# Kernel tuning notes

Hardware: AMD Instinct MI355X
Metric: run time of the kernel (lower is better)

## Reference

```python
import jax, jax.numpy as jnp
import numpy as np

B, IN, H = 16384, 1024, 1024


def setup_inputs() -> dict:
    key = jax.random.key(0)
    ks = jax.random.split(key, 7)
    s_in = 1.0 / np.sqrt(IN)
    s_h = 1.0 / np.sqrt(H)
    return {
        "x": jax.random.normal(ks[0], (B, IN), jnp.float32),
        "h0": jax.random.normal(ks[1], (B, H), jnp.float32),
        "c0": jax.random.normal(ks[2], (B, H), jnp.float32),
        # gate order along leading dim: f, i, o, g
        "wi": jax.random.uniform(ks[3], (4, H, IN), jnp.float32, -s_in, s_in),
        "bi": jax.random.uniform(ks[4], (4, H), jnp.float32, -s_in, s_in),
        "wh": jax.random.uniform(ks[5], (4, H, H), jnp.float32, -s_h, s_h),
        "bh": jax.random.uniform(ks[6], (4, H), jnp.float32, -s_h, s_h),
    }


def reference(x, h0, c0, wi, bi, wh, bh):
    # pre-activations for all 4 gates in two fused GEMMs: [b, 4, h]
    z = (jnp.einsum("bi,ghi->bgh", x, wi) + bi
         + jnp.einsum("bj,ghj->bgh", h0, wh) + bh)
    f = jax.nn.sigmoid(z[:, 0])   # forget gate
    i = jax.nn.sigmoid(z[:, 1])   # input gate
    o = jax.nn.sigmoid(z[:, 2])   # output gate
    g = jnp.tanh(z[:, 3])         # candidates
    ct = f * c0 + i * g
    ht = o * jnp.tanh(ct)
    return ht, ct
```

## Files before the change

### kernel.cpp

```cpp
#include <hip/hip_runtime.h>
#include <hip/hip_bf16.h>
#include <stdint.h>

#define B_ROWS 16384
#define K_DIM  2048
#define H_DIM  1024
#define N_DIM  4096
#define KB     (K_DIM * 2)
#define NT     (K_DIM / 64)
#define BUFSZ  65536u

using f32x4   = __attribute__((ext_vector_type(4))) float;
using f32x16  = __attribute__((ext_vector_type(16))) float;
using bf16x8  = __attribute__((ext_vector_type(8))) __bf16;

__device__ __forceinline__ unsigned short f2bf(float f) {
    union { float f; unsigned u; } v; v.f = f;
    unsigned r = v.u + 0x7fffu + ((v.u >> 16) & 1u);
    return (unsigned short)(r >> 16);
}

__device__ __forceinline__ void gload16(const void* g, const void* l) {
    __builtin_amdgcn_global_load_lds(
        (const __attribute__((address_space(1))) void*)g,
        (__attribute__((address_space(3))) void*)l,
        16, 0, 0);
}

__device__ __forceinline__ float rcp1p(float e) {
    return __builtin_amdgcn_rcpf(1.f + e);
}

__global__ void pack_a_kernel(const float* __restrict__ x, const float* __restrict__ h0,
                              unsigned short* __restrict__ A) {
    int tid = blockIdx.x * 256 + threadIdx.x;
    int64_t idx = (int64_t)tid * 4;
    int b = (int)(idx >> 11);
    int k = (int)(idx & 2047);
    const float* src = (k < 1024) ? (x + (int64_t)b * 1024 + k)
                                  : (h0 + (int64_t)b * 1024 + (k - 1024));
    float4 v = *(const float4*)src;
    ushort4 o;
    o.x = f2bf(v.x); o.y = f2bf(v.y); o.z = f2bf(v.z); o.w = f2bf(v.w);
    *(ushort4*)(A + idx) = o;
}

__global__ void pack_w_kernel(const float* __restrict__ wi, const float* __restrict__ wh,
                              const float* __restrict__ bi, const float* __restrict__ bh,
                              unsigned short* __restrict__ W, float* __restrict__ bias) {
    int tid = blockIdx.x * 256 + threadIdx.x;
    int64_t idx = (int64_t)tid * 4;
    int r = (int)(idx >> 11);
    int k = (int)(idx & 2047);
    int h = r >> 2, g = r & 3;
    const float* src = (k < 1024)
        ? (wi + (int64_t)g * 1048576 + (int64_t)h * 1024 + k)
        : (wh + (int64_t)g * 1048576 + (int64_t)h * 1024 + (k - 1024));
    float4 v = *(const float4*)src;
    ushort4 o;
    o.x = f2bf(v.x); o.y = f2bf(v.y); o.z = f2bf(v.z); o.w = f2bf(v.w);
    *(ushort4*)(W + idx) = o;
    if (k == 0) bias[r] = bi[g * 1024 + h] + bh[g * 1024 + h];
}


#define SCHED0  __builtin_amdgcn_sched_barrier(0)
#define FENCE   asm volatile("" ::: "memory")
#define BAR     __builtin_amdgcn_s_barrier()

#define PH_PRE  do { FENCE; BAR; \
                     asm volatile("s_waitcnt lgkmcnt(0)" ::: "memory"); \
                     SCHED0; __builtin_amdgcn_s_setprio(1); } while (0)
#define PH_POST_V do { __builtin_amdgcn_s_setprio(0); SCHED0; \
                       asm volatile("s_waitcnt vmcnt(4)" ::: "memory"); \
                       SCHED0; FENCE; BAR; } while (0)

__global__ __launch_bounds__(512, 2) void lstm_gemm_fused(
    const unsigned short* __restrict__ A, const unsigned short* __restrict__ W,
    const float* __restrict__ bias, const float* __restrict__ c0,
    float* __restrict__ ht, float* __restrict__ ct)
{
    __shared__ char sm[131072];

    const int tid = threadIdx.x;
    const int l   = tid & 63;
    const int w   = tid >> 6;
    const int wm  = w >> 2;
    const int wn  = w & 3;

    const int bid = blockIdx.x;
    const int nid = (bid & 7) * 128 + (bid >> 3);
    const int bm  = nid >> 4;
    const int bn  = nid & 15;

    f32x16 acc[4][2];
#pragma unroll
    for (int i = 0; i < 4; ++i)
#pragma unroll
        for (int j = 0; j < 2; ++j)
#pragma unroll
            for (int e = 0; e < 16; ++e) acc[i][j][e] = 0.f;

    const int srow = w * 16 + (l >> 2);
    const int scb  = ((l & 3) << 4) ^ (l & 32);
    const char* Asrc = (const char*)A + (size_t)(bm * 256 + srow) * KB + scb;
    const char* Wsrc = (const char*)W + (size_t)(bn * 256 + srow) * KB + scb;
    const uint32_t wL = (uint32_t)w * 1024u;

#define STAGE_A(KK, BOFF) do { \
    gload16(Asrc + (KK) * 64,            sm + (BOFF) + (KK) * 16384u + wL); \
    gload16(Asrc + (KK) * 64 + 128 * KB, sm + (BOFF) + (KK) * 16384u + 8192u + wL); \
} while (0)
#define STAGE_B(KK, BOFF) do { \
    gload16(Wsrc + (KK) * 64,            sm + (BOFF) + 32768u + (KK) * 16384u + wL); \
    gload16(Wsrc + (KK) * 64 + 128 * KB, sm + (BOFF) + 32768u + (KK) * 16384u + 8192u + wL); \
} while (0)

    const uint32_t sub   = ((uint32_t)(l >> 4) & 1u) * 1024u;
    const uint32_t lofA  = (uint32_t)(l & 15) * 64u + ((uint32_t)(l >> 5)) * 16u;
    const uint32_t xr    = (uint32_t)((l & 8) << 2);
    const uint32_t lane0 = sub + lofA + xr;
    const uint32_t lane1 = sub + lofA + (xr ^ 32u);
    const uint32_t ArdB  = (uint32_t)wm * 8192u;
    const uint32_t BrdB  = 32768u + (uint32_t)wn * 4096u;

    bf16x8 af[4][2], bf[2][2];

#define RD_PHASE(BOFF, KK) do { \
    const uint32_t cb_ = (BOFF) + (KK) * 16384u; \
    _Pragma("unroll") \
    for (int mf_ = 0; mf_ < 4; ++mf_) { \
        af[mf_][0] = *(const bf16x8*)(sm + cb_ + ArdB + mf_ * 2048u + lane0); \
        af[mf_][1] = *(const bf16x8*)(sm + cb_ + ArdB + mf_ * 2048u + lane1); \
    } \
    _Pragma("unroll") \
    for (int nf_ = 0; nf_ < 2; ++nf_) { \
        bf[nf_][0] = *(const bf16x8*)(sm + cb_ + BrdB + nf_ * 2048u + lane0); \
        bf[nf_][1] = *(const bf16x8*)(sm + cb_ + BrdB + nf_ * 2048u + lane1); \
    } \
} while (0)

#define MFMA16 do { \
    _Pragma("unroll") \
    for (int ks_ = 0; ks_ < 2; ++ks_) \
        _Pragma("unroll") \
        for (int mf_ = 0; mf_ < 4; ++mf_) \
            _Pragma("unroll") \
            for (int nf_ = 0; nf_ < 2; ++nf_) \
                acc[mf_][nf_] = __builtin_amdgcn_mfma_f32_32x32x16_bf16( \
                    af[mf_][ks_], bf[nf_][ks_], acc[mf_][nf_], 0, 0, 0); \
} while (0)

    STAGE_A(0, 0u); STAGE_B(0, 0u);
    STAGE_A(1, 0u); STAGE_B(1, 0u);
    Asrc += 128; Wsrc += 128;
    asm volatile("s_waitcnt vmcnt(4)" ::: "memory");
    SCHED0; FENCE; BAR;

#define DO_TILE(CUR, NXT) do { \
     \
    RD_PHASE(CUR, 0); \
    STAGE_A(0, NXT); STAGE_B(0, NXT); \
    PH_PRE; MFMA16; PH_POST_V; \
     \
    RD_PHASE(CUR, 1); \
    STAGE_A(1, NXT); STAGE_B(1, NXT); \
    PH_PRE; MFMA16; PH_POST_V; \
    Asrc += 128; Wsrc += 128; \
} while (0)

#pragma unroll 1
    for (int tt = 0; tt < NT; tt += 2) {
        DO_TILE(0u, BUFSZ);
        DO_TILE(BUFSZ, 0u);
    }

    asm volatile("s_waitcnt vmcnt(0) lgkmcnt(0)" ::: "memory");
    FENCE; BAR;

    float* ep = (float*)(void*)sm + w * 2176;
    const int hbase = bn * 64 + wn * 16;
    const int rbase = bm * 256 + wm * 128;
    const int rl = (l >> 5) * 4;
    const int cl = l & 31;

#pragma unroll
    for (int mf = 0; mf < 4; ++mf) {
#pragma unroll
        for (int nf = 0; nf < 2; ++nf)
#pragma unroll
            for (int g = 0; g < 4; ++g)
#pragma unroll
                for (int ri = 0; ri < 4; ++ri)
                    ep[(ri + g * 8 + rl) * 68 + nf * 32 + cl] = acc[mf][nf][g * 4 + ri];

#pragma unroll
        for (int it = 0; it < 8; ++it) {
            const int c   = it * 64 + l;
            const int row = c >> 4;
            const int hq  = c & 15;
            f32x4 z = *(const f32x4*)(ep + row * 68 + hq * 4);
            const int hg = hbase + hq;
            const float4 bz = ((const float4*)bias)[hg];
            const int brow = rbase + mf * 32 + row;

            float zf = z.x + bz.x;
            float zi = z.y + bz.y;
            float zo = z.z + bz.z;
            float zg = z.w + bz.w;

            float fg = rcp1p(__expf(-zf));
            float ig = rcp1p(__expf(-zi));
            float og = rcp1p(__expf(-zo));
            float gg = 2.f * rcp1p(__expf(-2.f * zg)) - 1.f;

            int64_t oi = (int64_t)brow * H_DIM + hg;
            float cc = fg * c0[oi] + ig * gg;
            float hh = og * (2.f * rcp1p(__expf(-2.f * cc)) - 1.f);
            ct[oi] = cc;
            ht[oi] = hh;
        }
    }
}

extern "C" void kernel_launch(void* const* d_in, const int* in_sizes, int n_in,
                              void* d_out, int out_size, void* d_ws, size_t ws_size,
                              hipStream_t stream) {
    const float* x  = (const float*)d_in[0];
    const float* h0 = (const float*)d_in[1];
    const float* c0 = (const float*)d_in[2];
    const float* wi = (const float*)d_in[3];
    const float* bi = (const float*)d_in[4];
    const float* wh = (const float*)d_in[5];
    const float* bh = (const float*)d_in[6];

    float* ht = (float*)d_out;
    float* ct = ht + (int64_t)B_ROWS * H_DIM;

    char* ws = (char*)d_ws;
    unsigned short* A  = (unsigned short*)ws;
    unsigned short* Wp = (unsigned short*)(ws + (64u << 20));
    float*          bs = (float*)(ws + (80u << 20));

    pack_a_kernel<<<32768, 256, 0, stream>>>(x, h0, A);
    pack_w_kernel<<<8192, 256, 0, stream>>>(wi, wh, bi, bh, Wp, bs);

    lstm_gemm_fused<<<1024, 512, 0, stream>>>(A, Wp, bs, c0, ht, ct);
}
```

Baseline: 344.0 us.

## Software-pipeline LDS fragment reads against MFMA with double-buffered A registers

Restructures the GEMM main loop so the LDS reads for the next k-phase are issued before the MFMAs of the current phase. Two alternating A-fragment register sets (aX/aY) make this possible, and there is now one barrier per phase instead of two. The explicit sched_barrier and lgkmcnt waits are removed, and an explicit prologue and epilogue drain the pipeline. It also adds a wave-parity XOR to the LDS swizzle, applied to both the global-to-LDS stores and the fragment reads, to reduce bank conflicts. The costs are higher register pressure, and tighter barrier ordering between buffer reuse and in-flight reads.

```diff
diff --git a/kernel.cpp b/kernel.cpp
--- a/kernel.cpp
+++ b/kernel.cpp
@@ -8,7 +8,8 @@
 #define N_DIM  4096
 #define KB     (K_DIM * 2)
 #define NT     (K_DIM / 64)
-#define BUFSZ  65536u
+#define BUF0   0u
+#define BUF1   65536u
 
 using f32x4   = __attribute__((ext_vector_type(4))) float;
 using f32x16  = __attribute__((ext_vector_type(16))) float;
@@ -64,16 +65,11 @@
 }
 
 
-#define SCHED0  __builtin_amdgcn_sched_barrier(0)
-#define FENCE   asm volatile("" ::: "memory")
-#define BAR     __builtin_amdgcn_s_barrier()
-
-#define PH_PRE  do { FENCE; BAR; \
-                     asm volatile("s_waitcnt lgkmcnt(0)" ::: "memory"); \
-                     SCHED0; __builtin_amdgcn_s_setprio(1); } while (0)
-#define PH_POST_V do { __builtin_amdgcn_s_setprio(0); SCHED0; \
-                       asm volatile("s_waitcnt vmcnt(4)" ::: "memory"); \
-                       SCHED0; FENCE; BAR; } while (0)
+#define FENCE asm volatile("" ::: "memory")
+#define BAR   __builtin_amdgcn_s_barrier()
+#define VM4   asm volatile("s_waitcnt vmcnt(4)" ::: "memory")
+#define SP1   __builtin_amdgcn_s_setprio(1)
+#define SP0   __builtin_amdgcn_s_setprio(0)
 
 __global__ __launch_bounds__(512, 2) void lstm_gemm_fused(
     const unsigned short* __restrict__ A, const unsigned short* __restrict__ W,
@@ -102,45 +98,48 @@
             for (int e = 0; e < 16; ++e) acc[i][j][e] = 0.f;
 
     const int srow = w * 16 + (l >> 2);
-    const int scb  = ((l & 3) << 4) ^ (l & 32);
+    const int scb  = (((l & 3) << 4) ^ (l & 32)) ^ ((w & 1) << 4);
     const char* Asrc = (const char*)A + (size_t)(bm * 256 + srow) * KB + scb;
     const char* Wsrc = (const char*)W + (size_t)(bn * 256 + srow) * KB + scb;
     const uint32_t wL = (uint32_t)w * 1024u;
 
-#define STAGE_A(KK, BOFF) do { \
+#define STAGE_AB(KK, BOFF) do { \
     gload16(Asrc + (KK) * 64,            sm + (BOFF) + (KK) * 16384u + wL); \
     gload16(Asrc + (KK) * 64 + 128 * KB, sm + (BOFF) + (KK) * 16384u + 8192u + wL); \
-} while (0)
-#define STAGE_B(KK, BOFF) do { \
     gload16(Wsrc + (KK) * 64,            sm + (BOFF) + 32768u + (KK) * 16384u + wL); \
     gload16(Wsrc + (KK) * 64 + 128 * KB, sm + (BOFF) + 32768u + (KK) * 16384u + 8192u + wL); \
 } while (0)
-
-    const uint32_t sub   = ((uint32_t)(l >> 4) & 1u) * 1024u;
-    const uint32_t lofA  = (uint32_t)(l & 15) * 64u + ((uint32_t)(l >> 5)) * 16u;
-    const uint32_t xr    = (uint32_t)((l & 8) << 2);
-    const uint32_t lane0 = sub + lofA + xr;
-    const uint32_t lane1 = sub + lofA + (xr ^ 32u);
+#define BUMP do { Asrc += 128; Wsrc += 128; } while (0)
+
+    const uint32_t sp    = (uint32_t)((l >> 4) & 1);
+    const uint32_t col0  = (((uint32_t)(l >> 5)) * 16u)
+                         ^ ((uint32_t)(l & 8) << 2) ^ (sp << 4);
+    const uint32_t lane0 = sp * 1024u + (uint32_t)(l & 15) * 64u + col0;
+    const uint32_t lane1 = lane0 ^ 32u;
     const uint32_t ArdB  = (uint32_t)wm * 8192u;
     const uint32_t BrdB  = 32768u + (uint32_t)wn * 4096u;
 
-    bf16x8 af[4][2], bf[2][2];
-
-#define RD_PHASE(BOFF, KK) do { \
+    bf16x8 aX[4][2], aY[4][2], bb[2][2];
+
+#define RD_A8(BOFF, KK, ARR) do { \
     const uint32_t cb_ = (BOFF) + (KK) * 16384u; \
     _Pragma("unroll") \
     for (int mf_ = 0; mf_ < 4; ++mf_) { \
-        af[mf_][0] = *(const bf16x8*)(sm + cb_ + ArdB + mf_ * 2048u + lane0); \
-        af[mf_][1] = *(const bf16x8*)(sm + cb_ + ArdB + mf_ * 2048u + lane1); \
+        ARR[mf_][0] = *(const bf16x8*)(sm + cb_ + ArdB + mf_ * 2048u + lane0); \
+        ARR[mf_][1] = *(const bf16x8*)(sm + cb_ + ArdB + mf_ * 2048u + lane1); \
     } \
+} while (0)
+#define RD_B4(BOFF, KK) do { \
+    const uint32_t cb_ = (BOFF) + (KK) * 16384u; \
     _Pragma("unroll") \
     for (int nf_ = 0; nf_ < 2; ++nf_) { \
-        bf[nf_][0] = *(const bf16x8*)(sm + cb_ + BrdB + nf_ * 2048u + lane0); \
-        bf[nf_][1] = *(const bf16x8*)(sm + cb_ + BrdB + nf_ * 2048u + lane1); \
+        bb[nf_][0] = *(const bf16x8*)(sm + cb_ + BrdB + nf_ * 2048u + lane0); \
+        bb[nf_][1] = *(const bf16x8*)(sm + cb_ + BrdB + nf_ * 2048u + lane1); \
     } \
 } while (0)
 
-#define MFMA16 do { \
+#define MFMA16(ARR) do { \
+    SP1; \
     _Pragma("unroll") \
     for (int ks_ = 0; ks_ < 2; ++ks_) \
         _Pragma("unroll") \
@@ -148,32 +147,48 @@
             _Pragma("unroll") \
             for (int nf_ = 0; nf_ < 2; ++nf_) \
                 acc[mf_][nf_] = __builtin_amdgcn_mfma_f32_32x32x16_bf16( \
-                    af[mf_][ks_], bf[nf_][ks_], acc[mf_][nf_], 0, 0, 0); \
-} while (0)
-
-    STAGE_A(0, 0u); STAGE_B(0, 0u);
-    STAGE_A(1, 0u); STAGE_B(1, 0u);
-    Asrc += 128; Wsrc += 128;
-    asm volatile("s_waitcnt vmcnt(4)" ::: "memory");
-    SCHED0; FENCE; BAR;
-
-#define DO_TILE(CUR, NXT) do { \
+                    ARR[mf_][ks_], bb[nf_][ks_], acc[mf_][nf_], 0, 0, 0); \
+    SP0; \
+} while (0)
+
+    STAGE_AB(0, BUF0); STAGE_AB(1, BUF0);
+    BUMP;
+    VM4; BAR; FENCE;
+    RD_A8(BUF0, 0, aX);
+    STAGE_AB(0, BUF1);
+    VM4; BAR; FENCE;
+    RD_B4(BUF0, 0);
+    RD_A8(BUF0, 1, aY);
+    STAGE_AB(1, BUF1);
+    BUMP;
+    MFMA16(aX);
+
+#define DO_TILE(AB, NB) do { \
      \
-    RD_PHASE(CUR, 0); \
-    STAGE_A(0, NXT); STAGE_B(0, NXT); \
-    PH_PRE; MFMA16; PH_POST_V; \
+    VM4; BAR; FENCE; \
+    RD_B4(NB, 1); \
+    RD_A8(AB, 0, aX); \
+    STAGE_AB(0, NB); \
+    MFMA16(aY); \
      \
-    RD_PHASE(CUR, 1); \
-    STAGE_A(1, NXT); STAGE_B(1, NXT); \
-    PH_PRE; MFMA16; PH_POST_V; \
-    Asrc += 128; Wsrc += 128; \
+    VM4; BAR; FENCE; \
+    RD_B4(AB, 0); \
+    RD_A8(AB, 1, aY); \
+    STAGE_AB(1, NB); \
+    BUMP; \
+    MFMA16(aX); \
 } while (0)
 
 #pragma unroll 1
-    for (int tt = 0; tt < NT; tt += 2) {
-        DO_TILE(0u, BUFSZ);
-        DO_TILE(BUFSZ, 0u);
+    for (int tt = 1; tt < NT - 1; tt += 2) {
+        DO_TILE(BUF1, BUF0);
+        DO_TILE(BUF0, BUF1);
     }
+    DO_TILE(BUF1, BUF0);
+
+    FENCE;
+    RD_B4(BUF1, 1);
+    MFMA16(aY);
 
     asm volatile("s_waitcnt vmcnt(0) lgkmcnt(0)" ::: "memory");
     FENCE; BAR;
```

Result: faster. 334.2 us (-2.9%).
